# Kernel tuning notes

Measured on AMD Instinct MI355X. Metric: run time of the kernel, lower is better.

Reference implementation:

```python
import jax, jax.numpy as jnp
import numpy as np

B, T, C, D = 8, 4096, 1024, 64  # batch, block_size, input_dim, output_dim


def setup_inputs() -> dict:
    key = jax.random.key(0)
    kx, kk, kq, kv = jax.random.split(key, 4)
    s = 1.0 / np.sqrt(C)  # nn.Linear default init range scale
    X = jax.random.normal(kx, (B, T, C), dtype=jnp.float32)
    Wk = jax.random.uniform(kk, (D, C), jnp.float32, -s, s) * 0.01  # key weight scaled by 0.01 per __post_init__
    Wq = jax.random.uniform(kq, (D, C), jnp.float32, -s, s)
    Wv = jax.random.uniform(kv, (D, C), jnp.float32, -s, s)
    return {"X": X, "Wk": Wk, "Wq": Wq, "Wv": Wv}


def reference(X, Wk, Wq, Wv):
    # bias-free linear projections (torch Linear: X @ W.T)
    keys = jnp.einsum('btc,dc->btd', X, Wk)
    queries = jnp.einsum('btc,dc->btd', X, Wq)
    values = jnp.einsum('btc,dc->btd', X, Wv)
    # scaled dot-product logits [B, T, T]
    logits = jnp.einsum('btd,bsd->bts', queries, keys) / jnp.sqrt(jnp.float32(D))
    causal = jnp.tril(jnp.ones((T, T), dtype=bool))
    logits = jnp.where(causal[None, :, :], logits, -jnp.inf)
    affinities = jax.nn.softmax(logits, axis=2)  # dropout_frac=0.0 -> identity
    return jnp.einsum('bts,bsd->btd', affinities, values)
```

## Files before the change

### kernel.cpp

```cpp
#include <hip/hip_runtime.h>


typedef short bf16x8 __attribute__((ext_vector_type(8)));
typedef short bf16x4 __attribute__((ext_vector_type(4)));
typedef float f32x4  __attribute__((ext_vector_type(4)));

static __device__ __forceinline__ short f2bf(float x) {
    union { float f; unsigned u; } v; v.f = x;
    return (short)((v.u + 0x7fffu + ((v.u >> 16) & 1u)) >> 16);
}

__global__ __launch_bounds__(256) void wconv_kernel(
    const float* __restrict__ Wk, const float* __restrict__ Wq,
    const float* __restrict__ Wv, short* __restrict__ Wc)
{
    const int i = (blockIdx.x * 256 + threadIdx.x) * 4;
    const int m = i >> 16;
    const int off = i & 65535;
    const float* src = (m == 0) ? Wk : (m == 1) ? Wq : Wv;
    const float s = (m == 1) ? 0.18033688f : 1.0f;
    f32x4 v = *(const f32x4*)(src + off);
    bf16x4 o;
#pragma unroll
    for (int r = 0; r < 4; ++r) o[r] = f2bf(v[r] * s);
    *(bf16x4*)(Wc + i) = o;
}

__global__ __launch_bounds__(256) void proj_kernel(
    const float* __restrict__ X,
    const short* __restrict__ Wc,
    short* __restrict__ Kb,
    short* __restrict__ Qb,
    short* __restrict__ Vt)
{
    const int tid  = threadIdx.x;
    const int w    = tid >> 6;
    const int lane = tid & 63;
    const int l15  = lane & 15;
    const int quad = lane >> 4;
    const int t0   = blockIdx.x * 128 + w * 32;

    const float* xA = X + (long)(t0 + l15) * 1024 + quad * 8;
    const float* xB = xA + 16 * 1024;
    const short* wb = Wc + (long)l15 * 1024 + quad * 8;

    f32x4 acc[2][12];
#pragma unroll
    for (int rt = 0; rt < 2; ++rt)
#pragma unroll
        for (int t = 0; t < 12; ++t) { acc[rt][t][0]=0.f; acc[rt][t][1]=0.f; acc[rt][t][2]=0.f; acc[rt][t][3]=0.f; }

    f32x4 ar[4][4];
#pragma unroll
    for (int d = 0; d < 3; ++d) {
        ar[d][0] = *(const f32x4*)(xA + d * 32);
        ar[d][1] = *(const f32x4*)(xA + d * 32 + 4);
        ar[d][2] = *(const f32x4*)(xB + d * 32);
        ar[d][3] = *(const f32x4*)(xB + d * 32 + 4);
    }

#pragma unroll 4
    for (int ks = 0; ks < 32; ++ks) {
        const int cur = ks & 3;
        if (ks + 3 < 32) {
            const int nxt = (ks + 3) & 3;
            ar[nxt][0] = *(const f32x4*)(xA + (ks + 3) * 32);
            ar[nxt][1] = *(const f32x4*)(xA + (ks + 3) * 32 + 4);
            ar[nxt][2] = *(const f32x4*)(xB + (ks + 3) * 32);
            ar[nxt][3] = *(const f32x4*)(xB + (ks + 3) * 32 + 4);
        }
        bf16x8 bw[12];
#pragma unroll
        for (int m = 0; m < 3; ++m)
#pragma unroll
            for (int dt = 0; dt < 4; ++dt)
                bw[m * 4 + dt] = *(const bf16x8*)(wb + m * 65536 + dt * 16384 + ks * 32);
        bf16x8 a0, a1;
#pragma unroll
        for (int j = 0; j < 4; ++j) {
            a0[j] = f2bf(ar[cur][0][j]); a0[j + 4] = f2bf(ar[cur][1][j]);
            a1[j] = f2bf(ar[cur][2][j]); a1[j + 4] = f2bf(ar[cur][3][j]);
        }
#pragma unroll
        for (int t = 0; t < 12; ++t) {
            acc[0][t] = __builtin_amdgcn_mfma_f32_16x16x32_bf16(a0, bw[t], acc[0][t], 0, 0, 0);
            acc[1][t] = __builtin_amdgcn_mfma_f32_16x16x32_bf16(a1, bw[t], acc[1][t], 0, 0, 0);
        }
    }

    const int bidx = t0 >> 12;
#pragma unroll
    for (int rt = 0; rt < 2; ++rt) {
        const int tf = t0 + rt * 16 + quad * 4;
#pragma unroll
        for (int dt = 0; dt < 4; ++dt) {
            const int d = dt * 16 + l15;
#pragma unroll
            for (int r = 0; r < 4; ++r) Kb[(long)(tf + r) * 64 + d] = f2bf(acc[rt][0 + dt][r]);
#pragma unroll
            for (int r = 0; r < 4; ++r) Qb[(long)(tf + r) * 64 + d] = f2bf(acc[rt][4 + dt][r]);
            bf16x4 pv;
#pragma unroll
            for (int r = 0; r < 4; ++r) pv[r] = f2bf(acc[rt][8 + dt][r]);
            *(bf16x4*)(Vt + ((long)bidx * 64 + d) * 4096 + (tf & 4095)) = pv;
        }
    }
}

__global__ __launch_bounds__(256) void flash_kernel(
    const short* __restrict__ Qb,
    const short* __restrict__ Kb,
    const short* __restrict__ Vt,
    float* __restrict__ Out)
{
    __shared__ __align__(16) char smem[33280];
    short* ps = (short*)smem;
    float* os = (float*)smem;
    float* ls = (float*)(smem + 32768);

    const int tid  = threadIdx.x;
    const int w    = tid >> 6;
    const int lane = tid & 63;
    const int l15  = lane & 15;
    const int quad = lane >> 4;
    const int b    = blockIdx.x & 7;
    const int tile = 127 - (blockIdx.x >> 3);
    const int t0   = tile * 32;

    const int nkb = (t0 >> 6) + 1;
    const int len = (nkb + 3) >> 2;
    const int kb0 = w * len;
    const int kb1 = (kb0 + len < nkb) ? (kb0 + len) : nkb;

    const short* Kbase = Kb + (long)b * 4096 * 64;
    const short* Vbase = Vt + (long)b * 64 * 4096;

    bf16x8 aq[2][2];
#pragma unroll
    for (int q2 = 0; q2 < 2; ++q2) {
        const long qoff = ((long)b * 4096 + t0 + q2 * 16 + l15) * 64;
        aq[q2][0] = *(const bf16x8*)(Qb + qoff + quad * 8);
        aq[q2][1] = *(const bf16x8*)(Qb + qoff + 32 + quad * 8);
    }

    bf16x8 bones;
#pragma unroll
    for (int j = 0; j < 8; ++j) bones[j] = (l15 == 0) ? (short)0x3F80 : (short)0;

    f32x4 o[2][4], lacc[2];
#pragma unroll
    for (int q2 = 0; q2 < 2; ++q2) {
        lacc[q2][0]=0.f; lacc[q2][1]=0.f; lacc[q2][2]=0.f; lacc[q2][3]=0.f;
#pragma unroll
        for (int dt = 0; dt < 4; ++dt) { o[q2][dt][0]=0.f; o[q2][dt][1]=0.f; o[q2][dt][2]=0.f; o[q2][dt][3]=0.f; }
    }

    bf16x8 kc[4][2], kn[4][2];
    if (kb0 < kb1) {
        const int s0 = kb0 << 6;
#pragma unroll
        for (int ct = 0; ct < 4; ++ct) {
            const short* kp = Kbase + (long)(s0 + ct * 16 + l15) * 64 + quad * 8;
            kc[ct][0] = *(const bf16x8*)(kp);
            kc[ct][1] = *(const bf16x8*)(kp + 32);
        }
    }

    for (int kb = kb0; kb < kb1; ++kb) {
        const int s0 = kb << 6;

        bf16x8 vf[4][2];
#pragma unroll
        for (int dt = 0; dt < 4; ++dt) {
            const short* vp = Vbase + (long)(dt * 16 + l15) * 4096 + s0 + quad * 8;
            vf[dt][0] = *(const bf16x8*)(vp);
            vf[dt][1] = *(const bf16x8*)(vp + 32);
        }
        if (kb + 1 < kb1) {
            const int sn = s0 + 64;
#pragma unroll
            for (int ct = 0; ct < 4; ++ct) {
                const short* kp = Kbase + (long)(sn + ct * 16 + l15) * 64 + quad * 8;
                kn[ct][0] = *(const bf16x8*)(kp);
                kn[ct][1] = *(const bf16x8*)(kp + 32);
            }
        }

        f32x4 st[2][4];
#pragma unroll
        for (int q2 = 0; q2 < 2; ++q2)
#pragma unroll
            for (int ct = 0; ct < 4; ++ct) {
                f32x4 z; z[0]=0.f; z[1]=0.f; z[2]=0.f; z[3]=0.f;
                z = __builtin_amdgcn_mfma_f32_16x16x32_bf16(aq[q2][0], kc[ct][0], z, 0, 0, 0);
                st[q2][ct] = __builtin_amdgcn_mfma_f32_16x16x32_bf16(aq[q2][1], kc[ct][1], z, 0, 0, 0);
            }

        if (kb == nkb - 1) {
#pragma unroll
            for (int q2 = 0; q2 < 2; ++q2)
#pragma unroll
                for (int ct = 0; ct < 4; ++ct) {
                    const int s = s0 + ct * 16 + l15;
#pragma unroll
                    for (int r = 0; r < 4; ++r)
                        if (s > t0 + q2 * 16 + quad * 4 + r) st[q2][ct][r] = -1e30f;
                }
        }

#pragma unroll
        for (int q2 = 0; q2 < 2; ++q2) {
            short* myps = ps + ((w << 1) | q2) * 1152;
#pragma unroll
            for (int ct = 0; ct < 4; ++ct)
#pragma unroll
                for (int r = 0; r < 4; ++r)
                    myps[(quad * 4 + r) * 72 + ct * 16 + l15] =
                        f2bf(__builtin_amdgcn_exp2f(st[q2][ct][r]));
        }

        bf16x8 ap[2][2];
#pragma unroll
        for (int q2 = 0; q2 < 2; ++q2) {
            short* myps = ps + ((w << 1) | q2) * 1152;
            ap[q2][0] = *(const bf16x8*)(myps + l15 * 72 + quad * 8);
            ap[q2][1] = *(const bf16x8*)(myps + l15 * 72 + 32 + quad * 8);
        }

#pragma unroll
        for (int q2 = 0; q2 < 2; ++q2) {
            lacc[q2] = __builtin_amdgcn_mfma_f32_16x16x32_bf16(ap[q2][0], bones, lacc[q2], 0, 0, 0);
            lacc[q2] = __builtin_amdgcn_mfma_f32_16x16x32_bf16(ap[q2][1], bones, lacc[q2], 0, 0, 0);
#pragma unroll
            for (int dt = 0; dt < 4; ++dt) {
                o[q2][dt] = __builtin_amdgcn_mfma_f32_16x16x32_bf16(ap[q2][0], vf[dt][0], o[q2][dt], 0, 0, 0);
                o[q2][dt] = __builtin_amdgcn_mfma_f32_16x16x32_bf16(ap[q2][1], vf[dt][1], o[q2][dt], 0, 0, 0);
            }
        }
#pragma unroll
        for (int ct = 0; ct < 4; ++ct) { kc[ct][0] = kn[ct][0]; kc[ct][1] = kn[ct][1]; }
    }

    __syncthreads();
#pragma unroll
    for (int q2 = 0; q2 < 2; ++q2) {
#pragma unroll
        for (int dt = 0; dt < 4; ++dt)
#pragma unroll
            for (int r = 0; r < 4; ++r)
                os[w * 2048 + (q2 * 16 + quad * 4 + r) * 64 + dt * 16 + l15] = o[q2][dt][r];
        if (l15 == 0) {
#pragma unroll
            for (int r = 0; r < 4; ++r) ls[w * 32 + q2 * 16 + quad * 4 + r] = lacc[q2][r];
        }
    }
    __syncthreads();

    const int row = tid >> 3, c0 = (tid & 7) * 8;
    f32x4 a0, a1; a0[0]=0.f;a0[1]=0.f;a0[2]=0.f;a0[3]=0.f; a1=a0;
    float lsum = 0.f;
#pragma unroll
    for (int w2 = 0; w2 < 4; ++w2) {
        f32x4 v0 = *(const f32x4*)(os + w2 * 2048 + row * 64 + c0);
        f32x4 v1 = *(const f32x4*)(os + w2 * 2048 + row * 64 + c0 + 4);
        a0[0]+=v0[0]; a0[1]+=v0[1]; a0[2]+=v0[2]; a0[3]+=v0[3];
        a1[0]+=v1[0]; a1[1]+=v1[1]; a1[2]+=v1[2]; a1[3]+=v1[3];
        lsum += ls[w2 * 32 + row];
    }
    const float inv = 1.0f / lsum;
    f32x4 r0, r1;
    r0[0]=a0[0]*inv; r0[1]=a0[1]*inv; r0[2]=a0[2]*inv; r0[3]=a0[3]*inv;
    r1[0]=a1[0]*inv; r1[1]=a1[1]*inv; r1[2]=a1[2]*inv; r1[3]=a1[3]*inv;
    float* op = Out + ((long)b * 4096 + t0 + row) * 64 + c0;
    *(f32x4*)(op)     = r0;
    *(f32x4*)(op + 4) = r1;
}

extern "C" void kernel_launch(void* const* d_in, const int* in_sizes, int n_in,
                              void* d_out, int out_size, void* d_ws, size_t ws_size,
                              hipStream_t stream) {
    const float* X  = (const float*)d_in[0];
    const float* Wk = (const float*)d_in[1];
    const float* Wq = (const float*)d_in[2];
    const float* Wv = (const float*)d_in[3];

    short* ws = (short*)d_ws;
    const long NE = (long)8 * 4096 * 64;
    short* Wc = ws;
    short* Qb = ws + 196608;
    short* Kb = Qb + NE;
    short* Vt = Kb + NE;

    wconv_kernel<<<192, 256, 0, stream>>>(Wk, Wq, Wv, Wc);
    proj_kernel<<<256, 256, 0, stream>>>(X, Wc, Kb, Qb, Vt);
    flash_kernel<<<1024, 256, 0, stream>>>(Qb, Kb, Vt, (float*)d_out);
}
```

Measured before the change: 305.4 us.

## Restructure projection with shared-memory X tiles and shrink flash LDS footprint

The projection kernel now has each block handle 32 rows, with the four waves splitting the 12 output column tiles. X is staged as bf16 in double-buffered shared memory using a cheaper perm-based pack, and the grid grows to 1024 blocks to raise occupancy and parallelism. The flash kernel's epilogue reduction now runs in two halves so its LDS shrinks from about 33KB to about 18.7KB, and it gets a launch bound of 3 for occupancy. The bf16 rounding is simplified to round-half-up, which slightly changes numerics and adds extra barriers in the epilogue.

```diff
diff --git a/kernel.cpp b/kernel.cpp
--- a/kernel.cpp
+++ b/kernel.cpp
@@ -8,6 +8,16 @@
 static __device__ __forceinline__ short f2bf(float x) {
     union { float f; unsigned u; } v; v.f = x;
     return (short)((v.u + 0x7fffu + ((v.u >> 16) & 1u)) >> 16);
+}
+
+static __device__ __forceinline__ bf16x8 pack8(f32x4 a, f32x4 b) {
+    union { f32x4 f; unsigned u[4]; } ua, ub; ua.f = a; ub.f = b;
+    union { bf16x8 s; unsigned u[4]; } r;
+    r.u[0] = __builtin_amdgcn_perm(ua.u[1] + 0x8000u, ua.u[0] + 0x8000u, 0x07060302u);
+    r.u[1] = __builtin_amdgcn_perm(ua.u[3] + 0x8000u, ua.u[2] + 0x8000u, 0x07060302u);
+    r.u[2] = __builtin_amdgcn_perm(ub.u[1] + 0x8000u, ub.u[0] + 0x8000u, 0x07060302u);
+    r.u[3] = __builtin_amdgcn_perm(ub.u[3] + 0x8000u, ub.u[2] + 0x8000u, 0x07060302u);
+    return r.s;
 }
 
 __global__ __launch_bounds__(256) void wconv_kernel(
@@ -26,97 +36,108 @@
     *(bf16x4*)(Wc + i) = o;
 }
 
-__global__ __launch_bounds__(256) void proj_kernel(
+__global__ __launch_bounds__(256, 4) void proj_kernel(
     const float* __restrict__ X,
     const short* __restrict__ Wc,
     short* __restrict__ Kb,
     short* __restrict__ Qb,
     short* __restrict__ Vt)
 {
+    __shared__ __align__(16) short xs[2][32 * 72];
     const int tid  = threadIdx.x;
     const int w    = tid >> 6;
     const int lane = tid & 63;
     const int l15  = lane & 15;
     const int quad = lane >> 4;
-    const int t0   = blockIdx.x * 128 + w * 32;
-
-    const float* xA = X + (long)(t0 + l15) * 1024 + quad * 8;
-    const float* xB = xA + 16 * 1024;
-    const short* wb = Wc + (long)l15 * 1024 + quad * 8;
-
-    f32x4 acc[2][12];
+    const int t0   = blockIdx.x * 32;
+
+    const int srow = tid >> 3, sseg = tid & 7;
+    const float* xp = X + (long)(t0 + srow) * 1024 + sseg * 8;
+    const int lw = srow * 72 + sseg * 8;
+
+    int mm[3], dd[3];
+    const short* wbp[3];
+#pragma unroll
+    for (int tt = 0; tt < 3; ++tt) {
+        const int g = w * 3 + tt;
+        mm[tt] = g >> 2; dd[tt] = (g & 3) * 16;
+        wbp[tt] = Wc + mm[tt] * 65536 + (long)(dd[tt] + l15) * 1024 + quad * 8;
+    }
+
+    f32x4 acc[2][3];
 #pragma unroll
     for (int rt = 0; rt < 2; ++rt)
 #pragma unroll
-        for (int t = 0; t < 12; ++t) { acc[rt][t][0]=0.f; acc[rt][t][1]=0.f; acc[rt][t][2]=0.f; acc[rt][t][3]=0.f; }
-
-    f32x4 ar[4][4];
-#pragma unroll
-    for (int d = 0; d < 3; ++d) {
-        ar[d][0] = *(const f32x4*)(xA + d * 32);
-        ar[d][1] = *(const f32x4*)(xA + d * 32 + 4);
-        ar[d][2] = *(const f32x4*)(xB + d * 32);
-        ar[d][3] = *(const f32x4*)(xB + d * 32 + 4);
-    }
-
-#pragma unroll 4
-    for (int ks = 0; ks < 32; ++ks) {
-        const int cur = ks & 3;
-        if (ks + 3 < 32) {
-            const int nxt = (ks + 3) & 3;
-            ar[nxt][0] = *(const f32x4*)(xA + (ks + 3) * 32);
-            ar[nxt][1] = *(const f32x4*)(xA + (ks + 3) * 32 + 4);
-            ar[nxt][2] = *(const f32x4*)(xB + (ks + 3) * 32);
-            ar[nxt][3] = *(const f32x4*)(xB + (ks + 3) * 32 + 4);
-        }
-        bf16x8 bw[12];
-#pragma unroll
-        for (int m = 0; m < 3; ++m)
-#pragma unroll
-            for (int dt = 0; dt < 4; ++dt)
-                bw[m * 4 + dt] = *(const bf16x8*)(wb + m * 65536 + dt * 16384 + ks * 32);
-        bf16x8 a0, a1;
-#pragma unroll
-        for (int j = 0; j < 4; ++j) {
-            a0[j] = f2bf(ar[cur][0][j]); a0[j + 4] = f2bf(ar[cur][1][j]);
-            a1[j] = f2bf(ar[cur][2][j]); a1[j + 4] = f2bf(ar[cur][3][j]);
-        }
-#pragma unroll
-        for (int t = 0; t < 12; ++t) {
-            acc[0][t] = __builtin_amdgcn_mfma_f32_16x16x32_bf16(a0, bw[t], acc[0][t], 0, 0, 0);
-            acc[1][t] = __builtin_amdgcn_mfma_f32_16x16x32_bf16(a1, bw[t], acc[1][t], 0, 0, 0);
-        }
+        for (int tt = 0; tt < 3; ++tt) { acc[rt][tt][0]=0.f; acc[rt][tt][1]=0.f; acc[rt][tt][2]=0.f; acc[rt][tt][3]=0.f; }
+
+    {
+        f32x4 g0 = *(const f32x4*)(xp);
+        f32x4 g1 = *(const f32x4*)(xp + 4);
+        *(bf16x8*)(&xs[0][lw]) = pack8(g0, g1);
+    }
+    __syncthreads();
+
+    for (int ks = 0; ks < 16; ++ks) {
+        const int buf = ks & 1;
+        f32x4 n0, n1;
+        if (ks < 15) {
+            n0 = *(const f32x4*)(xp + (ks + 1) * 64);
+            n1 = *(const f32x4*)(xp + (ks + 1) * 64 + 4);
+        }
+        bf16x8 bw[3][2];
+#pragma unroll
+        for (int tt = 0; tt < 3; ++tt)
+#pragma unroll
+            for (int kk = 0; kk < 2; ++kk)
+                bw[tt][kk] = *(const bf16x8*)(wbp[tt] + ks * 64 + kk * 32);
+#pragma unroll
+        for (int kk = 0; kk < 2; ++kk) {
+            bf16x8 a0 = *(const bf16x8*)(&xs[buf][l15 * 72 + kk * 32 + quad * 8]);
+            bf16x8 a1 = *(const bf16x8*)(&xs[buf][(16 + l15) * 72 + kk * 32 + quad * 8]);
+#pragma unroll
+            for (int tt = 0; tt < 3; ++tt) {
+                acc[0][tt] = __builtin_amdgcn_mfma_f32_16x16x32_bf16(a0, bw[tt][kk], acc[0][tt], 0, 0, 0);
+                acc[1][tt] = __builtin_amdgcn_mfma_f32_16x16x32_bf16(a1, bw[tt][kk], acc[1][tt], 0, 0, 0);
+            }
+        }
+        if (ks < 15) *(bf16x8*)(&xs[buf ^ 1][lw]) = pack8(n0, n1);
+        __syncthreads();
     }
 
     const int bidx = t0 >> 12;
 #pragma unroll
     for (int rt = 0; rt < 2; ++rt) {
         const int tf = t0 + rt * 16 + quad * 4;
-#pragma unroll
-        for (int dt = 0; dt < 4; ++dt) {
-            const int d = dt * 16 + l15;
-#pragma unroll
-            for (int r = 0; r < 4; ++r) Kb[(long)(tf + r) * 64 + d] = f2bf(acc[rt][0 + dt][r]);
-#pragma unroll
-            for (int r = 0; r < 4; ++r) Qb[(long)(tf + r) * 64 + d] = f2bf(acc[rt][4 + dt][r]);
-            bf16x4 pv;
-#pragma unroll
-            for (int r = 0; r < 4; ++r) pv[r] = f2bf(acc[rt][8 + dt][r]);
-            *(bf16x4*)(Vt + ((long)bidx * 64 + d) * 4096 + (tf & 4095)) = pv;
-        }
-    }
-}
-
-__global__ __launch_bounds__(256) void flash_kernel(
+        const int tl = tf & 4095;
+#pragma unroll
+        for (int tt = 0; tt < 3; ++tt) {
+            const int d = dd[tt] + l15;
+            if (mm[tt] == 0) {
+#pragma unroll
+                for (int r = 0; r < 4; ++r) Kb[(long)(tf + r) * 64 + d] = f2bf(acc[rt][tt][r]);
+            } else if (mm[tt] == 1) {
+#pragma unroll
+                for (int r = 0; r < 4; ++r) Qb[(long)(tf + r) * 64 + d] = f2bf(acc[rt][tt][r]);
+            } else {
+                bf16x4 pv;
+#pragma unroll
+                for (int r = 0; r < 4; ++r) pv[r] = f2bf(acc[rt][tt][r]);
+                *(bf16x4*)(Vt + ((long)bidx * 64 + d) * 4096 + tl) = pv;
+            }
+        }
+    }
+}
+
+__global__ __launch_bounds__(256, 3) void flash_kernel(
     const short* __restrict__ Qb,
     const short* __restrict__ Kb,
     const short* __restrict__ Vt,
     float* __restrict__ Out)
 {
-    __shared__ __align__(16) char smem[33280];
+    __shared__ __align__(16) char smem[18688];
     short* ps = (short*)smem;
     float* os = (float*)smem;
-    float* ls = (float*)(smem + 32768);
+    float* ls = (float*)(smem + 18432);
 
     const int tid  = threadIdx.x;
     const int w    = tid >> 6;
@@ -214,9 +235,11 @@
 #pragma unroll
             for (int ct = 0; ct < 4; ++ct)
 #pragma unroll
-                for (int r = 0; r < 4; ++r)
-                    myps[(quad * 4 + r) * 72 + ct * 16 + l15] =
-                        f2bf(__builtin_amdgcn_exp2f(st[q2][ct][r]));
+                for (int r = 0; r < 4; ++r) {
+                    union { float f; unsigned u; } pv;
+                    pv.f = __builtin_amdgcn_exp2f(st[q2][ct][r]);
+                    myps[(quad * 4 + r) * 72 + ct * 16 + l15] = (short)((pv.u + 0x8000u) >> 16);
+                }
         }
 
         bf16x8 ap[2][2];
@@ -241,39 +264,33 @@
         for (int ct = 0; ct < 4; ++ct) { kc[ct][0] = kn[ct][0]; kc[ct][1] = kn[ct][1]; }
     }
 
-    __syncthreads();
 #pragma unroll
     for (int q2 = 0; q2 < 2; ++q2) {
+        __syncthreads();
 #pragma unroll
         for (int dt = 0; dt < 4; ++dt)
 #pragma unroll
             for (int r = 0; r < 4; ++r)
-                os[w * 2048 + (q2 * 16 + quad * 4 + r) * 64 + dt * 16 + l15] = o[q2][dt][r];
+                os[w * 1024 + (quad * 4 + r) * 64 + dt * 16 + l15] = o[q2][dt][r];
         if (l15 == 0) {
 #pragma unroll
-            for (int r = 0; r < 4; ++r) ls[w * 32 + q2 * 16 + quad * 4 + r] = lacc[q2][r];
-        }
-    }
-    __syncthreads();
-
-    const int row = tid >> 3, c0 = (tid & 7) * 8;
-    f32x4 a0, a1; a0[0]=0.f;a0[1]=0.f;a0[2]=0.f;a0[3]=0.f; a1=a0;
-    float lsum = 0.f;
-#pragma unroll
-    for (int w2 = 0; w2 < 4; ++w2) {
-        f32x4 v0 = *(const f32x4*)(os + w2 * 2048 + row * 64 + c0);
-        f32x4 v1 = *(const f32x4*)(os + w2 * 2048 + row * 64 + c0 + 4);
-        a0[0]+=v0[0]; a0[1]+=v0[1]; a0[2]+=v0[2]; a0[3]+=v0[3];
-        a1[0]+=v1[0]; a1[1]+=v1[1]; a1[2]+=v1[2]; a1[3]+=v1[3];
-        lsum += ls[w2 * 32 + row];
-    }
-    const float inv = 1.0f / lsum;
-    f32x4 r0, r1;
-    r0[0]=a0[0]*inv; r0[1]=a0[1]*inv; r0[2]=a0[2]*inv; r0[3]=a0[3]*inv;
-    r1[0]=a1[0]*inv; r1[1]=a1[1]*inv; r1[2]=a1[2]*inv; r1[3]=a1[3]*inv;
-    float* op = Out + ((long)b * 4096 + t0 + row) * 64 + c0;
-    *(f32x4*)(op)     = r0;
-    *(f32x4*)(op + 4) = r1;
+            for (int r = 0; r < 4; ++r) ls[w * 16 + quad * 4 + r] = lacc[q2][r];
+        }
+        __syncthreads();
+
+        const int row = tid >> 4, c4 = (tid & 15) * 4;
+        f32x4 a; a[0]=0.f; a[1]=0.f; a[2]=0.f; a[3]=0.f;
+        float lsum = 0.f;
+#pragma unroll
+        for (int w2 = 0; w2 < 4; ++w2) {
+            f32x4 v = *(const f32x4*)(os + w2 * 1024 + row * 64 + c4);
+            a[0]+=v[0]; a[1]+=v[1]; a[2]+=v[2]; a[3]+=v[3];
+            lsum += ls[w2 * 16 + row];
+        }
+        const float inv = 1.0f / lsum;
+        f32x4 res; res[0]=a[0]*inv; res[1]=a[1]*inv; res[2]=a[2]*inv; res[3]=a[3]*inv;
+        *(f32x4*)(Out + ((long)b * 4096 + t0 + q2 * 16 + row) * 64 + c4) = res;
+    }
 }
 
 extern "C" void kernel_launch(void* const* d_in, const int* in_sizes, int n_in,
@@ -292,6 +309,6 @@
     short* Vt = Kb + NE;
 
     wconv_kernel<<<192, 256, 0, stream>>>(Wk, Wq, Wv, Wc);
-    proj_kernel<<<256, 256, 0, stream>>>(X, Wc, Kb, Qb, Vt);
+    proj_kernel<<<1024, 256, 0, stream>>>(X, Wc, Kb, Qb, Vt);
     flash_kernel<<<1024, 256, 0, stream>>>(Qb, Kb, Vt, (float*)d_out);
 }
```

New measurement: 317.4 us. +3.9%, slower.
